# Optimization experiments

Measured on AMD Instinct MI355X. Metric: run time of the kernel, lower is better.

Reference implementation:

```python
import jax, jax.numpy as jnp
import numpy as np

N_NODES = 100000
N_EDGES = 1600000
IN_CH = 128
TYPE_EMB = 32
OUT_CH = 128
N_REL = 8
N_BASES = 8
N_NTYPES = 8
FEAT = IN_CH + TYPE_EMB  # 160, RGCNConv input dim after concat


def setup_inputs() -> dict:
    key = jax.random.key(0)
    ks = jax.random.split(key, 9)
    x = jax.random.normal(ks[0], (N_NODES, IN_CH), dtype=jnp.float32)
    node_type_ids = jax.random.randint(ks[1], (N_NODES,), 0, N_NTYPES)
    edge_index = jax.random.randint(ks[2], (2, N_EDGES), 0, N_NODES)
    edge_type = jax.random.randint(ks[3], (N_EDGES,), 0, N_REL)
    emb_table = jax.random.normal(ks[4], (N_NTYPES, TYPE_EMB), dtype=jnp.float32)
    bases = jax.random.normal(ks[5], (N_BASES, FEAT, OUT_CH), dtype=jnp.float32) * (1.0 / np.sqrt(FEAT))
    comp = jax.random.normal(ks[6], (N_REL, N_BASES), dtype=jnp.float32) * (1.0 / np.sqrt(N_BASES))
    root_w = jax.random.normal(ks[7], (FEAT, OUT_CH), dtype=jnp.float32) * (1.0 / np.sqrt(FEAT))
    bias = jnp.zeros((OUT_CH,), dtype=jnp.float32)
    return {"x": x, "node_type_ids": node_type_ids, "edge_index": edge_index,
            "edge_type": edge_type, "emb_table": emb_table, "bases": bases,
            "comp": comp, "root_w": root_w, "bias": bias}


def reference(x, node_type_ids, edge_index, edge_type, emb_table, bases, comp, root_w, bias):
    N = x.shape[0]
    # node-type embedding lookup + concat
    h = jnp.concatenate([x, emb_table[node_type_ids]], axis=1)  # [N, FEAT]
    # basis decomposition: per-relation weights [R, FEAT, OUT]
    weight = jnp.einsum('rb,bio->rio', comp, bases)
    src, dst = edge_index[0], edge_index[1]
    h_src = h[src]  # [E, FEAT] -- dominant gather
    # root/self transform + bias
    out = h @ root_w + bias
    # PyG RGCNConv default aggr='mean': per-relation mean over incoming edges, summed across relations
    for r in range(weight.shape[0]):
        m = (edge_type == r).astype(h.dtype)  # [E]
        s = jax.ops.segment_sum(h_src * m[:, None], dst, num_segments=N)  # [N, FEAT]
        c = jax.ops.segment_sum(m, dst, num_segments=N)                    # [N]
        mean_r = s / jnp.maximum(c, 1.0)[:, None]
        out = out + mean_r @ weight[r]
    # dropout is identity in eval mode
    return jax.nn.relu(out)
```

## Files before the change

### kernel.cpp

```cpp
#include <hip/hip_runtime.h>

#define NN 100000
#define NE 1600000
#define INC 128
#define TE 32
#define OC 128
#define NR 8
#define NBASES 8
#define FT 160
#define KP 168
#define KW 160
#define TN 64
#define NBKT 1563
#define NCH 128
#define EPB 12500
#define CAP 1536

typedef float f32x4 __attribute__((ext_vector_type(4)));
typedef __bf16 bf16x8 __attribute__((ext_vector_type(8)));

__device__ __forceinline__ unsigned f2bf1(float f) {
    unsigned u = __float_as_uint(f);
    return (u + 0x7fffu + ((u >> 16) & 1u)) >> 16;
}

__device__ __forceinline__ int bscan_excl(int v, int* tmp) {
    int tid = threadIdx.x;
    tmp[tid] = v; __syncthreads();
#pragma unroll
    for (int d = 1; d < 256; d <<= 1) {
        int t = (tid >= d) ? tmp[tid - d] : 0;
        __syncthreads();
        tmp[tid] += t;
        __syncthreads();
    }
    return tmp[tid] - v;
}

__global__ __launch_bounds__(256) void k_prep(
    const float* __restrict__ x, const int* __restrict__ nt,
    const float* __restrict__ emb, const float* __restrict__ comp,
    const float* __restrict__ bases, const float* __restrict__ rootw,
    const int* __restrict__ ei,
    unsigned short* __restrict__ h, unsigned short* __restrict__ Wt,
    int* __restrict__ ghist) {
    __shared__ int hist[NBKT];
    int tid = threadIdx.x;
    int b = blockIdx.x;
    if (b < NCH) {
        for (int j = tid; j < NBKT; j += 256) hist[j] = 0;
        __syncthreads();
        int e0 = b * EPB;
#pragma unroll
        for (int k = 0; k < 49; k++) {
            int i = k * 256 + tid;
            if (i < EPB) atomicAdd(&hist[ei[NE + e0 + i] >> 6], 1);
        }
        __syncthreads();
        int* g = ghist + (size_t)b * NBKT;
        for (int j = tid; j < NBKT; j += 256) g[j] = hist[j];
        return;
    }
    int idx = (b - NCH) * 256 + tid;
    if (idx < 9 * 128 * KW) {
        int ridx = idx / (128 * KW);
        int rem  = idx % (128 * KW);
        int o = rem / KW;
        int k = rem % KW;
        float v;
        if (ridx < NR) {
            v = 0.f;
#pragma unroll
            for (int bb = 0; bb < NBASES; bb++)
                v += comp[ridx * NBASES + bb] * bases[(bb * FT + k) * OC + o];
        } else {
            v = rootw[k * OC + o];
        }
        Wt[idx] = (unsigned short)f2bf1(v);
    }
    if (idx < NN * 20) {
        int n = idx / 20, c = idx % 20;
        f32x4 v0, v1;
        if (c < 16) {
            const float* p = x + (size_t)n * INC + c * 8;
            v0 = *(const f32x4*)p; v1 = *(const f32x4*)(p + 4);
        } else {
            int tt = nt[n];
            const float* p = emb + tt * TE + (c - 16) * 8;
            v0 = *(const f32x4*)p; v1 = *(const f32x4*)(p + 4);
        }
        uint4 o;
        o.x = f2bf1(v0.x) | (f2bf1(v0.y) << 16);
        o.y = f2bf1(v0.z) | (f2bf1(v0.w) << 16);
        o.z = f2bf1(v1.x) | (f2bf1(v1.y) << 16);
        o.w = f2bf1(v1.z) | (f2bf1(v1.w) << 16);
        *(uint4*)(h + (size_t)n * FT + c * 8) = o;
    }
}

__global__ void k_total(const int* __restrict__ ghist, int* __restrict__ total) {
    int j = blockIdx.x * 256 + threadIdx.x;
    if (j >= NBKT) return;
    int s = 0;
#pragma unroll 8
    for (int b = 0; b < NCH; b++) s += ghist[(size_t)b * NBKT + j];
    total[j] = s;
}

__global__ void k_scanTot(const int* __restrict__ total, int* __restrict__ bstart) {
    __shared__ int tmp[256];
    int tid = threadIdx.x, s = 0, i0 = tid * 7;
#pragma unroll
    for (int i = 0; i < 7; i++) { int j = i0 + i; if (j < NBKT) s += total[j]; }
    int run = bscan_excl(s, tmp);
#pragma unroll
    for (int i = 0; i < 7; i++) { int j = i0 + i; if (j < NBKT) { bstart[j] = run; run += total[j]; } }
    if (tid == 0) bstart[NBKT] = NE;
}

__global__ void k_offsets(int* __restrict__ ghist, const int* __restrict__ bstart) {
    int j = blockIdx.x * 256 + threadIdx.x;
    if (j >= NBKT) return;
    int run = bstart[j];
#pragma unroll 4
    for (int b = 0; b < NCH; b++) {
        int v = ghist[(size_t)b * NBKT + j];
        ghist[(size_t)b * NBKT + j] = run;
        run += v;
    }
}

__global__ __launch_bounds__(256) void k_scatter(const int* __restrict__ ei, const int* __restrict__ et,
                                                 const int* __restrict__ ghist, unsigned* __restrict__ slots) {
    __shared__ int cur[NBKT];
    int tid = threadIdx.x, b = blockIdx.x;
    for (int j = tid; j < NBKT; j += 256) cur[j] = ghist[(size_t)b * NBKT + j];
    __syncthreads();
    int e0 = b * EPB;
#pragma unroll
    for (int k = 0; k < 49; k++) {
        int i = k * 256 + tid;
        if (i < EPB) {
            int e = e0 + i;
            int s = ei[e], d = ei[NE + e], r = et[e];
            int pos = atomicAdd(&cur[d >> 6], 1);
            slots[pos] = (unsigned)s | ((unsigned)r << 17) | ((unsigned)(d & 63) << 20);
        }
    }
}

__global__ __launch_bounds__(256, 4) void k_mega(
    const unsigned short* __restrict__ h, const float* __restrict__ bias,
    const unsigned short* __restrict__ Wt, const int* __restrict__ bstart,
    const unsigned* __restrict__ slots, float* __restrict__ out) {
    __shared__ unsigned short featmem[TN * KP];
    __shared__ unsigned sl[CAP];
    __shared__ unsigned pkl[512];

    const int tid = threadIdx.x;
    const int lane = tid & 63;
    const int wave = tid >> 6;
    const int j = blockIdx.x;
    const int n0 = j * TN;

    unsigned* sl_in = reinterpret_cast<unsigned*>(featmem);
    int* hist = reinterpret_cast<int*>(featmem) + CAP;
    int* tmp  = reinterpret_cast<int*>(featmem) + CAP + 512;

    int s0 = bstart[j];
    int m = bstart[j + 1] - s0; if (m > CAP) m = CAP;
    for (int i = tid; i < m; i += 256) sl_in[i] = slots[s0 + i];
    for (int k = tid; k < 512; k += 256) hist[k] = 0;
    __syncthreads();
    for (int i = tid; i < m; i += 256) {
        unsigned v = sl_in[i];
        atomicAdd(&hist[((v >> 17) & 7u) * 64u + ((v >> 20) & 63u)], 1);
    }
    __syncthreads();
    int v0 = hist[2 * tid], v1 = hist[2 * tid + 1];
    int ex = bscan_excl(v0 + v1, tmp);
    pkl[2 * tid]     = (unsigned)ex | ((unsigned)v0 << 16);
    pkl[2 * tid + 1] = (unsigned)(ex + v0) | ((unsigned)v1 << 16);
    hist[2 * tid] = ex; hist[2 * tid + 1] = ex + v0;
    __syncthreads();
    for (int i = tid; i < m; i += 256) {
        unsigned v = sl_in[i];
        int p = atomicAdd(&hist[((v >> 17) & 7u) * 64u + ((v >> 20) & 63u)], 1);
        sl[p] = v & 0x03F1FFFFu;
    }
    __syncthreads();

    for (int i = tid; i < TN * 20; i += 256) {
        int nl = i / 20, c = i % 20, n = n0 + nl;
        uint4 v = (uint4){0u, 0u, 0u, 0u};
        if (n < NN) v = *reinterpret_cast<const uint4*>(h + (size_t)n * FT + c * 8);
        *reinterpret_cast<uint4*>(&featmem[nl * KP + c * 8]) = v;
    }

    f32x4 acc[8];
#pragma unroll
    for (int t = 0; t < 8; t++) acc[t] = (f32x4){0.f, 0.f, 0.f, 0.f};

    auto mfma_pass = [&](int ridx) {
        const unsigned short* fA = featmem + (lane & 15) * KP + ((lane >> 4) * 8);
        const unsigned short* gB = Wt + (size_t)ridx * 128 * KW
                                   + (wave * 32 + (lane & 15)) * KW + ((lane >> 4) * 8);
#pragma unroll
        for (int kc = 0; kc < 5; kc++) {
            bf16x8 a0 = *reinterpret_cast<const bf16x8*>(fA + 0 * 16 * KP + kc * 32);
            bf16x8 a1 = *reinterpret_cast<const bf16x8*>(fA + 1 * 16 * KP + kc * 32);
            bf16x8 a2 = *reinterpret_cast<const bf16x8*>(fA + 2 * 16 * KP + kc * 32);
            bf16x8 a3 = *reinterpret_cast<const bf16x8*>(fA + 3 * 16 * KP + kc * 32);
#pragma unroll
            for (int ct = 0; ct < 2; ct++) {
                bf16x8 b = *reinterpret_cast<const bf16x8*>(gB + ct * 16 * KW + kc * 32);
                acc[0 * 2 + ct] = __builtin_amdgcn_mfma_f32_16x16x32_bf16(a0, b, acc[0 * 2 + ct], 0, 0, 0);
                acc[1 * 2 + ct] = __builtin_amdgcn_mfma_f32_16x16x32_bf16(a1, b, acc[1 * 2 + ct], 0, 0, 0);
                acc[2 * 2 + ct] = __builtin_amdgcn_mfma_f32_16x16x32_bf16(a2, b, acc[2 * 2 + ct], 0, 0, 0);
                acc[3 * 2 + ct] = __builtin_amdgcn_mfma_f32_16x16x32_bf16(a3, b, acc[3 * 2 + ct], 0, 0, 0);
            }
        }
    };

    __syncthreads();
    mfma_pass(8);

    const int g = tid >> 4, l = tid & 15;
    const unsigned* hw = reinterpret_cast<const unsigned*>(h);
    for (int r = 0; r < NR; r++) {
        __syncthreads();
        int b0 = r * 64 + 4 * g;
        unsigned pa = pkl[b0], pd = pkl[b0 + 3];
        int sbeg = (int)(pa & 0xffffu);
        int send = (int)(pd & 0xffffu) + (int)(pd >> 16);
        float sa[10];
#pragma unroll
        for (int i = 0; i < 10; i++) sa[i] = 0.f;
        float run = 0.f;
        for (int e = sbeg; e < send; e += 4) {
            unsigned w[4][5];
            int dl[4];
#pragma unroll
            for (int u = 0; u < 4; u++) {
                int eu = e + u; if (eu >= send) eu = send - 1;
                unsigned v = sl[eu];
                const unsigned* hp = hw + (size_t)(v & 0x1FFFFu) * 80 + l;
#pragma unroll
                for (int c = 0; c < 5; c++) w[u][c] = hp[c * 16];
                dl[u] = (int)((v >> 20) & 63u);
            }
#pragma unroll
            for (int u = 0; u < 4; u++) {
                if (e + u < send) {
#pragma unroll
                    for (int c = 0; c < 5; c++) {
                        sa[2 * c]     += __uint_as_float(w[u][c] << 16);
                        sa[2 * c + 1] += __uint_as_float(w[u][c] & 0xFFFF0000u);
                    }
                    run += 1.f;
                    bool last = (e + u + 1 >= send);
                    int ndl = last ? -1 : (int)((sl[e + u + 1] >> 20) & 63u);
                    if (last || ndl != dl[u]) {
                        float inv = 1.0f / run;
                        unsigned* fp = reinterpret_cast<unsigned*>(featmem + dl[u] * KP) + l;
#pragma unroll
                        for (int c = 0; c < 5; c++)
                            fp[c * 16] = f2bf1(sa[2 * c] * inv) | (f2bf1(sa[2 * c + 1] * inv) << 16);
#pragma unroll
                        for (int i = 0; i < 10; i++) sa[i] = 0.f;
                        run = 0.f;
                    }
                }
            }
        }
#pragma unroll
        for (int q = 0; q < 4; q++) {
            if ((pkl[b0 + q] >> 16) == 0u) {
                unsigned* fp = reinterpret_cast<unsigned*>(featmem + (4 * g + q) * KP) + l;
#pragma unroll
                for (int c = 0; c < 5; c++) fp[c * 16] = 0u;
            }
        }
        __syncthreads();
        mfma_pass(r);
    }

    const int rq = lane >> 4;
#pragma unroll
    for (int ct = 0; ct < 2; ct++) {
        int col = wave * 32 + ct * 16 + (lane & 15);
        float bv = bias[col];
#pragma unroll
        for (int rt = 0; rt < 4; rt++) {
#pragma unroll
            for (int i = 0; i < 4; i++) {
                int n = n0 + rt * 16 + rq * 4 + i;
                if (n < NN) {
                    float v = acc[rt * 2 + ct][i] + bv;
                    out[(size_t)n * OC + col] = v > 0.f ? v : 0.f;
                }
            }
        }
    }
}

extern "C" void kernel_launch(void* const* d_in, const int* in_sizes, int n_in,
                              void* d_out, int out_size, void* d_ws, size_t ws_size,
                              hipStream_t stream) {
    const float* x     = (const float*)d_in[0];
    const int*   ntype = (const int*)d_in[1];
    const int*   ei    = (const int*)d_in[2];
    const int*   et    = (const int*)d_in[3];
    const float* emb   = (const float*)d_in[4];
    const float* bases = (const float*)d_in[5];
    const float* comp  = (const float*)d_in[6];
    const float* rootw = (const float*)d_in[7];
    const float* bias  = (const float*)d_in[8];
    float* out = (float*)d_out;

    char* ws = (char*)d_ws;
    unsigned short* Wt     = (unsigned short*)(ws);
    unsigned short* h      = (unsigned short*)(ws + 368640);
    int*            ghist  = (int*)(ws + 32368640);
    int*            total  = (int*)(ws + 33168896);
    int*            bstart = (int*)(ws + 33175296);
    unsigned*       slots  = (unsigned*)(ws + 33181696);

    k_prep   <<<NCH + 7813, 256, 0, stream>>>(x, ntype, emb, comp, bases, rootw, ei, h, Wt, ghist);
    k_total  <<<7,    256, 0, stream>>>(ghist, total);
    k_scanTot<<<1,    256, 0, stream>>>(total, bstart);
    k_offsets<<<7,    256, 0, stream>>>(ghist, bstart);
    k_scatter<<<NCH,  256, 0, stream>>>(ei, et, ghist, slots);
    k_mega   <<<NBKT, 256, 0, stream>>>(h, bias, Wt, bstart, slots, out);
}
```

Measured before the change: 350.3 us.

## Vectorize gather loads, use segment boundaries, packed bf16 convert, raise occupancy

The edge-gather loop now reads each source row as one 16-byte load per lane plus one dword, instead of five strided dword loads. Destination changes are detected by comparing against precomputed per-node segment boundaries, so the next slot no longer has to be reloaded and the local dst bits can be stripped from slots. Accumulation uses packed float2 vectors, the mean is stored with v_cvt_pk_bf16_f32 and a fast reciprocal, and launch bounds ask for 5 blocks per CU. The costs are a changed per-lane column layout in LDS and possible register pressure or spilling at the higher occupancy target.

```diff
diff --git a/kernel.cpp b/kernel.cpp
--- a/kernel.cpp
+++ b/kernel.cpp
@@ -17,11 +17,21 @@
 #define CAP 1536
 
 typedef float f32x4 __attribute__((ext_vector_type(4)));
+typedef float f32x2 __attribute__((ext_vector_type(2)));
 typedef __bf16 bf16x8 __attribute__((ext_vector_type(8)));
 
 __device__ __forceinline__ unsigned f2bf1(float f) {
     unsigned u = __float_as_uint(f);
     return (u + 0x7fffu + ((u >> 16) & 1u)) >> 16;
+}
+
+__device__ __forceinline__ float bflo(unsigned u) { return __uint_as_float(u << 16); }
+__device__ __forceinline__ float bfhi(unsigned u) { return __uint_as_float(u & 0xFFFF0000u); }
+
+__device__ __forceinline__ unsigned cvtpk(float a, float b) {
+    unsigned r;
+    asm("v_cvt_pk_bf16_f32 %0, %1, %2" : "=v"(r) : "v"(a), "v"(b));
+    return r;
 }
 
 __device__ __forceinline__ int bscan_excl(int v, int* tmp) {
@@ -149,7 +159,7 @@
     }
 }
 
-__global__ __launch_bounds__(256, 4) void k_mega(
+__global__ __launch_bounds__(256, 5) void k_mega(
     const unsigned short* __restrict__ h, const float* __restrict__ bias,
     const unsigned short* __restrict__ Wt, const int* __restrict__ bstart,
     const unsigned* __restrict__ slots, float* __restrict__ out) {
@@ -186,7 +196,7 @@
     for (int i = tid; i < m; i += 256) {
         unsigned v = sl_in[i];
         int p = atomicAdd(&hist[((v >> 17) & 7u) * 64u + ((v >> 20) & 63u)], 1);
-        sl[p] = v & 0x03F1FFFFu;
+        sl[p] = v & 0x1FFFFu;
     }
     __syncthreads();
 
@@ -230,44 +240,50 @@
     for (int r = 0; r < NR; r++) {
         __syncthreads();
         int b0 = r * 64 + 4 * g;
-        unsigned pa = pkl[b0], pd = pkl[b0 + 3];
-        int sbeg = (int)(pa & 0xffffu);
-        int send = (int)(pd & 0xffffu) + (int)(pd >> 16);
-        float sa[10];
-#pragma unroll
-        for (int i = 0; i < 10; i++) sa[i] = 0.f;
+        unsigned pk1 = pkl[b0 + 1], pk2 = pkl[b0 + 2], pk3 = pkl[b0 + 3];
+        int sbeg = (int)(pkl[b0] & 0xffffu);
+        int e1 = (int)(pk1 & 0xffffu);
+        int e2 = (int)(pk2 & 0xffffu);
+        int e3 = (int)(pk3 & 0xffffu);
+        int send = e3 + (int)(pk3 >> 16);
+        f32x2 sa[5];
+#pragma unroll
+        for (int i = 0; i < 5; i++) sa[i] = (f32x2){0.f, 0.f};
         float run = 0.f;
         for (int e = sbeg; e < send; e += 4) {
-            unsigned w[4][5];
-            int dl[4];
+            uint4 wv[4]; unsigned tv[4];
 #pragma unroll
             for (int u = 0; u < 4; u++) {
                 int eu = e + u; if (eu >= send) eu = send - 1;
-                unsigned v = sl[eu];
-                const unsigned* hp = hw + (size_t)(v & 0x1FFFFu) * 80 + l;
-#pragma unroll
-                for (int c = 0; c < 5; c++) w[u][c] = hp[c * 16];
-                dl[u] = (int)((v >> 20) & 63u);
+                const unsigned* hp = hw + (size_t)sl[eu] * 80;
+                wv[u] = *reinterpret_cast<const uint4*>(hp + 4 * l);
+                tv[u] = hp[64 + l];
             }
 #pragma unroll
             for (int u = 0; u < 4; u++) {
                 if (e + u < send) {
-#pragma unroll
-                    for (int c = 0; c < 5; c++) {
-                        sa[2 * c]     += __uint_as_float(w[u][c] << 16);
-                        sa[2 * c + 1] += __uint_as_float(w[u][c] & 0xFFFF0000u);
-                    }
+                    sa[0] += (f32x2){bflo(wv[u].x), bfhi(wv[u].x)};
+                    sa[1] += (f32x2){bflo(wv[u].y), bfhi(wv[u].y)};
+                    sa[2] += (f32x2){bflo(wv[u].z), bfhi(wv[u].z)};
+                    sa[3] += (f32x2){bflo(wv[u].w), bfhi(wv[u].w)};
+                    sa[4] += (f32x2){bflo(tv[u]), bfhi(tv[u])};
                     run += 1.f;
-                    bool last = (e + u + 1 >= send);
-                    int ndl = last ? -1 : (int)((sl[e + u + 1] >> 20) & 63u);
-                    if (last || ndl != dl[u]) {
-                        float inv = 1.0f / run;
-                        unsigned* fp = reinterpret_cast<unsigned*>(featmem + dl[u] * KP) + l;
-#pragma unroll
-                        for (int c = 0; c < 5; c++)
-                            fp[c * 16] = f2bf1(sa[2 * c] * inv) | (f2bf1(sa[2 * c + 1] * inv) << 16);
-#pragma unroll
-                        for (int i = 0; i < 10; i++) sa[i] = 0.f;
+                    int nx = e + u + 1;
+                    if (nx == e1 || nx == e2 || nx == e3 || nx == send) {
+                        int q = (e + u >= e1) + (e + u >= e2) + (e + u >= e3);
+                        float inv = __builtin_amdgcn_rcpf(run);
+                        f32x2 m0 = sa[0] * inv, m1 = sa[1] * inv, m2 = sa[2] * inv,
+                              m3 = sa[3] * inv, m4 = sa[4] * inv;
+                        unsigned* fp = reinterpret_cast<unsigned*>(featmem + (4 * g + q) * KP);
+                        uint4 o;
+                        o.x = cvtpk(m0.x, m0.y);
+                        o.y = cvtpk(m1.x, m1.y);
+                        o.z = cvtpk(m2.x, m2.y);
+                        o.w = cvtpk(m3.x, m3.y);
+                        *reinterpret_cast<uint4*>(fp + 4 * l) = o;
+                        fp[64 + l] = cvtpk(m4.x, m4.y);
+#pragma unroll
+                        for (int i = 0; i < 5; i++) sa[i] = (f32x2){0.f, 0.f};
                         run = 0.f;
                     }
                 }
@@ -276,9 +292,9 @@
 #pragma unroll
         for (int q = 0; q < 4; q++) {
             if ((pkl[b0 + q] >> 16) == 0u) {
-                unsigned* fp = reinterpret_cast<unsigned*>(featmem + (4 * g + q) * KP) + l;
-#pragma unroll
-                for (int c = 0; c < 5; c++) fp[c * 16] = 0u;
+                unsigned* fp = reinterpret_cast<unsigned*>(featmem + (4 * g + q) * KP);
+                *reinterpret_cast<uint4*>(fp + 4 * l) = (uint4){0u, 0u, 0u, 0u};
+                fp[64 + l] = 0u;
             }
         }
         __syncthreads();
```

After: 355.7 us. No clear change (+1.6%).
